# Performance work log

Measured on AMD Instinct MI355X. Metric: run time of the kernel, lower is better.

## Reference

```python
import jax, jax.numpy as jnp
import numpy as np

NEG = -100.0
M2M, M2I, M2D, I2M, I2I, D2M, D2D = range(7)
LOG_Q = float(np.log(0.25))


def _d_chain(fM, aM2D, aD2D):
    """Sequential delete-state recurrence along motif axis k.
    fD[k] = logaddexp(aM2D[k-1] + fM[k-1], aD2D[k-1] + fD[k-1]), fD[0] = NEG.
    fM: (B, K+1); aM2D, aD2D: (B, K+1). Returns (B, K+1)."""
    B, Kp1 = fM.shape
    K = Kp1 - 1

    def step(fd_prev, inp):
        am, ad, fm = inp  # each (B,)
        fd = jnp.logaddexp(am + fm, ad + fd_prev)
        return fd, fd

    init = jnp.full((B,), NEG, dtype=fM.dtype)
    _, fds = jax.lax.scan(step, init, (aM2D[:, :K].T, aD2D[:, :K].T, fM[:, :K].T))
    return jnp.concatenate([init[:, None], fds.T], axis=1)


def _profile_hmm_loss(a, e, x):
    """pHMM forward algorithm (log-space). a: (B,K+1,7), e: (B,K,4), x: (B,L) int.
    Returns -log P(x) per batch element, shape (B,)."""
    B, Kp1, _ = a.shape
    K = Kp1 - 1

    fM0 = jnp.full((B, Kp1), NEG, dtype=a.dtype).at[:, 0].set(0.0)
    fI0 = jnp.full((B, Kp1), NEG, dtype=a.dtype)
    fD0 = _d_chain(fM0, a[:, :, M2D], a[:, :, D2D])

    def l_step(carry, x_l):
        fM, fI, fD = carry
        # emission for symbol x_l at each match state k: (B, K)
        esel = jnp.take_along_axis(e, x_l[:, None, None].astype(jnp.int32), axis=2)[:, :, 0]
        prev = jnp.logaddexp(
            jnp.logaddexp(a[:, :K, M2M] + fM[:, :K], a[:, :K, I2M] + fI[:, :K]),
            a[:, :K, D2M] + fD[:, :K],
        )
        fM_new = jnp.concatenate([jnp.full((B, 1), NEG, dtype=a.dtype), esel + prev], axis=1)
        fI_new = LOG_Q + jnp.logaddexp(a[:, :, M2I] + fM, a[:, :, I2I] + fI)
        fD_new = _d_chain(fM_new, a[:, :, M2D], a[:, :, D2D])
        return (fM_new, fI_new, fD_new), None

    (fM, fI, fD), _ = jax.lax.scan(l_step, (fM0, fI0, fD0), x.T)

    final = jnp.stack(
        [fM[:, K] + a[:, K, M2M], fI[:, K] + a[:, K, I2M], fD[:, K] + a[:, K, D2M]],
        axis=1,
    )
    return -jax.nn.logsumexp(final, axis=1)


def _kld_loss(mus, logvars):
    return -0.5 * jnp.sum(1.0 + logvars - mus * mus - jnp.exp(logvars), axis=1)


def setup_inputs() -> dict:
    key = jax.random.key(0)
    k1, k2, k3, k4, k5 = jax.random.split(key, 5)
    B, K, L, E = 4096, 64, 128, 16
    batch_input = jax.random.randint(k1, (B, L), 0, 4, dtype=jnp.int32)
    transition_probs = jax.random.normal(k2, (B, K + 1, 7), dtype=jnp.float32)
    emission_probs = jax.random.normal(k3, (B, K, 4), dtype=jnp.float32)
    mus = jax.random.normal(k4, (B, E), dtype=jnp.float32)
    logvars = jax.random.normal(k5, (B, E), dtype=jnp.float32)
    return {
        "batch_input": batch_input,
        "transition_probs": transition_probs,
        "emission_probs": emission_probs,
        "mus": mus,
        "logvars": logvars,
    }


def reference(batch_input, transition_probs, emission_probs, mus, logvars):
    beta = 1.0
    recon = jnp.mean(_profile_hmm_loss(transition_probs, emission_probs, batch_input))
    kld = jnp.mean(_kld_loss(mus, logvars))
    return recon + beta * kld
```

## Files before the change

### kernel.cpp

```cpp
#include <hip/hip_runtime.h>
#include <math.h>


namespace {

constexpr float kLog2e = 1.4426950408889634f;
constexpr float kLn2   = 0.6931471805599453f;

__device__ __forceinline__ float fexp(float x) {
    return __builtin_amdgcn_exp2f(x * kLog2e);
}

template <int CTRL, bool BC>
__device__ __forceinline__ float dppf(float old, float src) {
    int r = __builtin_amdgcn_update_dpp(__builtin_bit_cast(int, old),
                                        __builtin_bit_cast(int, src),
                                        CTRL, 0xF, 0xF, BC);
    return __builtin_bit_cast(float, r);
}

__global__ __launch_bounds__(256) void phmm_vae_kernel(
    const int* __restrict__ xg,
    const float* __restrict__ ag,
    const float* __restrict__ eg,
    const float* __restrict__ mug,
    const float* __restrict__ lvg,
    float* __restrict__ out, unsigned* __restrict__ wsc, float* __restrict__ wsf,
    int B)
{
    const int tid  = threadIdx.x;
    const int lane = tid & 63;
    const int wv   = tid >> 6;
    const int b    = (blockIdx.x << 2) + wv;

    __shared__ float part[4];
    float contrib = 0.0f;

    if (b < B) {
        const float* ab = ag + (size_t)b * (65 * 7);
        const float* eb = eg + (size_t)b * (64 * 4);
        const int*   xb = xg + (size_t)b * 128;

        const int j = lane;
        const float AjM2D  = fexp(ab[j * 7 + 2]);
        const float d      = fexp(ab[j * 7 + 6]);
        const float A1M2M  = fexp(ab[(j + 1) * 7 + 0]);
        const float QA1M2I = 0.25f * fexp(ab[(j + 1) * 7 + 1]);
        const float A1I2M  = fexp(ab[(j + 1) * 7 + 3]);
        const float QA1I2I = 0.25f * fexp(ab[(j + 1) * 7 + 4]);
        const float A1D2M  = fexp(ab[(j + 1) * 7 + 5]);
        const float A0M2M  = fexp(ab[0]);
        const float QA0M2I = 0.25f * fexp(ab[1]);
        const float A0I2M  = fexp(ab[3]);
        const float D0     = 0.25f * fexp(ab[4]);

        float4 ev = *reinterpret_cast<const float4*>(eb + j * 4);
        const float E0 = fexp(ev.x), E1 = fexp(ev.y);
        const float E2 = fexp(ev.z), E3 = fexp(ev.w);

        const int xlo = xb[lane];
        const int xhi = xb[64 + lane];
        const unsigned long long b0lo = __ballot(xlo & 1);
        const unsigned long long b1lo = __ballot(xlo & 2);
        const unsigned long long b0hi = __ballot(xhi & 1);
        const unsigned long long b1hi = __ballot(xhi & 2);

        const float V1 = d;
        const float V2 = V1 * dppf<0x111, false>(1.0f, V1);
        const float V4 = V2 * dppf<0x112, false>(1.0f, V2);
        const float V8 = V4 * dppf<0x114, false>(1.0f, V4);
        float Q = d;
        Q *= dppf<0x111, false>(1.0f, Q);
        Q *= dppf<0x112, false>(1.0f, Q);
        Q *= dppf<0x114, false>(1.0f, Q);
        Q *= dppf<0x118, false>(1.0f, Q);
        const int   row  = lane >> 4;
        const float Q47  = __shfl(Q, 47, 64);
        const float QmA  = (row == 1 || row == 3) ? Q : 0.0f;
        const float QmB  = (row == 2) ? Q : ((row == 3) ? Q * Q47 : 0.0f);

        auto dchain = [&](float fMn, float f0) -> float {
            float fMp = dppf<0x138, false>(f0, fMn);
            float y = AjM2D * fMp;
            y = fmaf(V1,  dppf<0x111, true>(y, y), y);
            y = fmaf(V2,  dppf<0x112, true>(y, y), y);
            y = fmaf(V4,  dppf<0x114, true>(y, y), y);
            y = fmaf(V8,  dppf<0x118, true>(y, y), y);
            y = fmaf(QmA, dppf<0x142, true>(y, y), y);
            y = fmaf(QmB, dppf<0x143, true>(y, y), y);
            return y;
        };

        auto esel_of = [&](unsigned long long m0, unsigned long long m1,
                           int sh) -> float {
            int bit0 = (int)(m0 >> sh) & 1;
            int bit1 = (int)(m1 >> sh) & 1;
            float eA = bit0 ? E1 : E0;
            float eB = bit0 ? E3 : E2;
            return bit1 ? eB : eA;
        };

        float fM = 0.0f, fI = 0.0f;
        float fD = dchain(0.0f, 1.0f);
        float LS = 0.0f;
        float fI0v;

        auto stepf = [&](float esel, float p0) {
            float pl = fmaf(A1M2M, fM, fmaf(A1I2M, fI, A1D2M * fD));
            float prev = dppf<0x138, false>(p0, pl);
            float fMn = esel * prev;
            fI = fmaf(QA1M2I, fM, QA1I2I * fI);
            fD = dchain(fMn, 0.0f);
            fM = fMn;
        };

        auto rescale = [&]() {
            float m = fmaxf(fmaxf(fM, fI), fD);
            m = fmaxf(m, dppf<0xB1,  true>(m, m));
            m = fmaxf(m, dppf<0x4E,  true>(m, m));
            m = fmaxf(m, dppf<0x141, true>(m, m));
            m = fmaxf(m, dppf<0x140, true>(m, m));
            int mb = __builtin_bit_cast(int, m);
            unsigned u0 = (unsigned)__builtin_amdgcn_readlane(mb, 0);
            unsigned u1 = (unsigned)__builtin_amdgcn_readlane(mb, 16);
            unsigned u2 = (unsigned)__builtin_amdgcn_readlane(mb, 32);
            unsigned u3 = (unsigned)__builtin_amdgcn_readlane(mb, 48);
            unsigned ua = u0 > u1 ? u0 : u1;
            unsigned ub = u2 > u3 ? u2 : u3;
            unsigned um = ua > ub ? ua : ub;
            int ee = (int)(um >> 23);
            float r = __builtin_bit_cast(float, (unsigned)(254 - ee) << 23);
            LS += (float)(ee - 127);
            fM *= r; fI *= r; fD *= r; fI0v *= r;
        };

        stepf(esel_of(b0lo, b1lo, 0), A0M2M);
        fI0v = QA0M2I;

        for (int l = 1; l < 64; ++l) {
            stepf(esel_of(b0lo, b1lo, l), A0I2M * fI0v);
            fI0v *= D0;
            if ((l & 7) == 7) rescale();
        }
        for (int l = 64; l < 128; ++l) {
            stepf(esel_of(b0hi, b1hi, l - 64), A0I2M * fI0v);
            fI0v *= D0;
            if ((l & 7) == 7) rescale();
        }

        float F = fmaf(A1M2M, fM, fmaf(A1I2M, fI, A1D2M * fD));
        float loss = -(__builtin_amdgcn_logf(F) + LS) * kLn2;

        float kt = 0.0f;
        if (lane < 16) {
            float mu = mug[(size_t)b * 16 + lane];
            float lv = lvg[(size_t)b * 16 + lane];
            kt = 1.0f + lv - mu * mu - fexp(lv);
        }
        kt += __shfl_xor(kt, 1, 64);
        kt += __shfl_xor(kt, 2, 64);
        kt += __shfl_xor(kt, 4, 64);
        kt += __shfl_xor(kt, 8, 64);
        float kldb = __shfl(-0.5f * kt, 0, 64);

        contrib = (loss + kldb) * (1.0f / 4096.0f);
    }

    if (lane == 63) part[wv] = (b < B) ? contrib : 0.0f;
    __syncthreads();
    if (tid == 0) {
        float bs = part[0] + part[1] + part[2] + part[3];
        const float    poisonf = __builtin_bit_cast(float, 0xAAAAAAAAu);
        atomicAdd(&wsf[1], bs);
        __threadfence();
        unsigned old = atomicAdd(&wsc[0], 1u);
        if (old == 0xAAAAAAAAu + (unsigned)(gridDim.x - 1)) {
            __threadfence();
            float total = atomicAdd(&wsf[1], 0.0f);
            out[0] = total - poisonf;
        }
    }
}

}

extern "C" void kernel_launch(void* const* d_in, const int* in_sizes, int n_in,
                              void* d_out, int out_size, void* d_ws, size_t ws_size,
                              hipStream_t stream) {
    const int*   x  = (const int*)d_in[0];
    const float* a  = (const float*)d_in[1];
    const float* e  = (const float*)d_in[2];
    const float* mu = (const float*)d_in[3];
    const float* lv = (const float*)d_in[4];
    float* out = (float*)d_out;

    const int B = in_sizes[0] / 128;
    const int grid = (B + 3) / 4;

    phmm_vae_kernel<<<grid, 256, 0, stream>>>(x, a, e, mu, lv, out,
                                              (unsigned*)d_ws, (float*)d_ws, B);
}
```

Measured before the change: 110.1 us.

## Fold delete-chain into match recurrence with inline-asm DPP scan and two-kernel reduction

Reformulates the per-step recurrence so the delete-state scan acts on the previous match input, with emissions and the M2D weight premultiplied into per-symbol constants. This takes the dchain off the dependency path between steps and carries the combined next-step value `pl` instead. The prefix scan is written as inline assembly with fused DPP multiply/fma ops, and lane masks are built into the scan coefficients. The atomic-counter final reduction is replaced by per-block partial sums plus a second tiny reduce kernel, which adds a kernel launch and relies on hand-placed s_nop hazards.

```diff
diff --git a/kernel.cpp b/kernel.cpp
--- a/kernel.cpp
+++ b/kernel.cpp
@@ -25,8 +25,7 @@
     const float* __restrict__ eg,
     const float* __restrict__ mug,
     const float* __restrict__ lvg,
-    float* __restrict__ out, unsigned* __restrict__ wsc, float* __restrict__ wsf,
-    int B)
+    float* __restrict__ partials, int B)
 {
     const int tid  = threadIdx.x;
     const int lane = tid & 63;
@@ -42,13 +41,13 @@
         const int*   xb = xg + (size_t)b * 128;
 
         const int j = lane;
-        const float AjM2D  = fexp(ab[j * 7 + 2]);
-        const float d      = fexp(ab[j * 7 + 6]);
+        const float a2  = ab[j * 7 + 2];
+        const float a6  = ab[j * 7 + 6];
+        const float a5  = ab[(j + 1) * 7 + 5];
         const float A1M2M  = fexp(ab[(j + 1) * 7 + 0]);
         const float QA1M2I = 0.25f * fexp(ab[(j + 1) * 7 + 1]);
         const float A1I2M  = fexp(ab[(j + 1) * 7 + 3]);
         const float QA1I2I = 0.25f * fexp(ab[(j + 1) * 7 + 4]);
-        const float A1D2M  = fexp(ab[(j + 1) * 7 + 5]);
         const float A0M2M  = fexp(ab[0]);
         const float QA0M2I = 0.25f * fexp(ab[1]);
         const float A0I2M  = fexp(ab[3]);
@@ -65,91 +64,110 @@
         const unsigned long long b0hi = __ballot(xhi & 1);
         const unsigned long long b1hi = __ballot(xhi & 2);
 
-        const float V1 = d;
+        const float a5p = dppf<0x138, false>(0.0f, a5);
+        const float dh  = fexp(a6 + a5 - a5p);
+        const float wM2D = fexp(a2 + a5);
+        const float C0 = wM2D * dppf<0x138, false>(0.0f, E0);
+        const float C1 = wM2D * dppf<0x138, false>(0.0f, E1);
+        const float C2 = wM2D * dppf<0x138, false>(0.0f, E2);
+        const float C3 = wM2D * dppf<0x138, false>(0.0f, E3);
+
+        const float V1 = dh;
         const float V2 = V1 * dppf<0x111, false>(1.0f, V1);
         const float V4 = V2 * dppf<0x112, false>(1.0f, V2);
         const float V8 = V4 * dppf<0x114, false>(1.0f, V4);
-        float Q = d;
+        const float V1m = (lane >= 1)  ? V1 : 0.0f;
+        const float V2m = (lane >= 2)  ? V2 : 0.0f;
+        const float V4m = (lane >= 4)  ? V4 : 0.0f;
+        const float V8m = (lane >= 8)  ? V8 : 0.0f;
+        float Q = dh;
         Q *= dppf<0x111, false>(1.0f, Q);
         Q *= dppf<0x112, false>(1.0f, Q);
         Q *= dppf<0x114, false>(1.0f, Q);
         Q *= dppf<0x118, false>(1.0f, Q);
-        const int   row  = lane >> 4;
-        const float Q47  = __shfl(Q, 47, 64);
-        const float QmA  = (row == 1 || row == 3) ? Q : 0.0f;
-        const float QmB  = (row == 2) ? Q : ((row == 3) ? Q * Q47 : 0.0f);
-
-        auto dchain = [&](float fMn, float f0) -> float {
-            float fMp = dppf<0x138, false>(f0, fMn);
-            float y = AjM2D * fMp;
-            y = fmaf(V1,  dppf<0x111, true>(y, y), y);
-            y = fmaf(V2,  dppf<0x112, true>(y, y), y);
-            y = fmaf(V4,  dppf<0x114, true>(y, y), y);
-            y = fmaf(V8,  dppf<0x118, true>(y, y), y);
-            y = fmaf(QmA, dppf<0x142, true>(y, y), y);
-            y = fmaf(QmB, dppf<0x143, true>(y, y), y);
+        const int   row = lane >> 4;
+        const float Q47 = __shfl(Q, 47, 64);
+        const float QmA = (row == 1 || row == 3) ? Q : 0.0f;
+        const float QmB = (row == 2) ? Q : ((row == 3) ? Q * Q47 : 0.0f);
+
+        auto scan_asm = [&](float prev, float Cs) -> float {
+            float y;
+            asm("s_nop 1\n\t"
+                "v_mul_f32_dpp %0, %1, %2 wave_shr:1 row_mask:0xf bank_mask:0xf bound_ctrl:0\n\t"
+                "s_nop 1\n\t"
+                "v_fmac_f32_dpp %0, %0, %3 row_shr:1 row_mask:0xf bank_mask:0xf bound_ctrl:0\n\t"
+                "s_nop 1\n\t"
+                "v_fmac_f32_dpp %0, %0, %4 row_shr:2 row_mask:0xf bank_mask:0xf bound_ctrl:0\n\t"
+                "s_nop 1\n\t"
+                "v_fmac_f32_dpp %0, %0, %5 row_shr:4 row_mask:0xf bank_mask:0xf bound_ctrl:0\n\t"
+                "s_nop 1\n\t"
+                "v_fmac_f32_dpp %0, %0, %6 row_shr:8 row_mask:0xf bank_mask:0xf bound_ctrl:0\n\t"
+                "s_nop 1\n\t"
+                "v_fmac_f32_dpp %0, %0, %7 row_bcast:15 row_mask:0xf bank_mask:0xf bound_ctrl:0\n\t"
+                "s_nop 1\n\t"
+                "v_fmac_f32_dpp %0, %0, %8 row_bcast:31 row_mask:0xf bank_mask:0xf bound_ctrl:0"
+                : "=&v"(y)
+                : "v"(prev), "v"(Cs), "v"(V1m), "v"(V2m), "v"(V4m), "v"(V8m),
+                  "v"(QmA), "v"(QmB));
             return y;
         };
 
-        auto esel_of = [&](unsigned long long m0, unsigned long long m1,
-                           int sh) -> float {
-            int bit0 = (int)(m0 >> sh) & 1;
-            int bit1 = (int)(m1 >> sh) & 1;
-            float eA = bit0 ? E1 : E0;
-            float eB = bit0 ? E3 : E2;
-            return bit1 ? eB : eA;
-        };
+        float y0 = (lane == 0) ? wM2D : 0.0f;
+        y0 = fmaf(V1m, dppf<0x111, true>(0.0f, y0), y0);
+        y0 = fmaf(V2m, dppf<0x112, true>(0.0f, y0), y0);
+        y0 = fmaf(V4m, dppf<0x114, true>(0.0f, y0), y0);
+        y0 = fmaf(V8m, dppf<0x118, true>(0.0f, y0), y0);
+        y0 = fmaf(QmA, dppf<0x142, true>(0.0f, y0), y0);
+        y0 = fmaf(QmB, dppf<0x143, true>(0.0f, y0), y0);
 
         float fM = 0.0f, fI = 0.0f;
-        float fD = dchain(0.0f, 1.0f);
+        float pl = y0;
+        float fI0v = 0.0f;
         float LS = 0.0f;
-        float fI0v;
-
-        auto stepf = [&](float esel, float p0) {
-            float pl = fmaf(A1M2M, fM, fmaf(A1I2M, fI, A1D2M * fD));
-            float prev = dppf<0x138, false>(p0, pl);
-            float fMn = esel * prev;
+
+#pragma unroll 8
+        for (int l = 0; l < 128; ++l) {
+            const unsigned long long m0 = (l < 64) ? b0lo : b0hi;
+            const unsigned long long m1 = (l < 64) ? b1lo : b1hi;
+            const int sh = l & 63;
+            const int bit0 = (int)(m0 >> sh) & 1;
+            const int bit1 = (int)(m1 >> sh) & 1;
+            const float Es = bit1 ? (bit0 ? E3 : E2) : (bit0 ? E1 : E0);
+            const float Cs = bit1 ? (bit0 ? C3 : C2) : (bit0 ? C1 : C0);
+
+            const float p0v = (l == 0) ? A0M2M : A0I2M * fI0v;
+            const float prev = dppf<0x138, false>(p0v, pl);
+            const float fMn = Es * prev;
+            const float z = scan_asm(prev, Cs);
             fI = fmaf(QA1M2I, fM, QA1I2I * fI);
-            fD = dchain(fMn, 0.0f);
             fM = fMn;
-        };
-
-        auto rescale = [&]() {
-            float m = fmaxf(fmaxf(fM, fI), fD);
-            m = fmaxf(m, dppf<0xB1,  true>(m, m));
-            m = fmaxf(m, dppf<0x4E,  true>(m, m));
-            m = fmaxf(m, dppf<0x141, true>(m, m));
-            m = fmaxf(m, dppf<0x140, true>(m, m));
-            int mb = __builtin_bit_cast(int, m);
-            unsigned u0 = (unsigned)__builtin_amdgcn_readlane(mb, 0);
-            unsigned u1 = (unsigned)__builtin_amdgcn_readlane(mb, 16);
-            unsigned u2 = (unsigned)__builtin_amdgcn_readlane(mb, 32);
-            unsigned u3 = (unsigned)__builtin_amdgcn_readlane(mb, 48);
-            unsigned ua = u0 > u1 ? u0 : u1;
-            unsigned ub = u2 > u3 ? u2 : u3;
-            unsigned um = ua > ub ? ua : ub;
-            int ee = (int)(um >> 23);
-            float r = __builtin_bit_cast(float, (unsigned)(254 - ee) << 23);
-            LS += (float)(ee - 127);
-            fM *= r; fI *= r; fD *= r; fI0v *= r;
-        };
-
-        stepf(esel_of(b0lo, b1lo, 0), A0M2M);
-        fI0v = QA0M2I;
-
-        for (int l = 1; l < 64; ++l) {
-            stepf(esel_of(b0lo, b1lo, l), A0I2M * fI0v);
-            fI0v *= D0;
-            if ((l & 7) == 7) rescale();
+            pl = fmaf(A1M2M, fM, fmaf(A1I2M, fI, z));
+            fI0v = (l == 0) ? QA0M2I : fI0v * D0;
+
+            if ((l & 7) == 7) {
+                float m = fmaxf(fmaxf(fM, fI), pl);
+                m = fmaxf(m, dppf<0xB1,  true>(0.0f, m));
+                m = fmaxf(m, dppf<0x4E,  true>(0.0f, m));
+                m = fmaxf(m, dppf<0x141, true>(0.0f, m));
+                m = fmaxf(m, dppf<0x140, true>(0.0f, m));
+                m = fmaxf(m, 1e-35f);
+                int mb = __builtin_bit_cast(int, m);
+                unsigned u0 = (unsigned)__builtin_amdgcn_readlane(mb, 0);
+                unsigned u1 = (unsigned)__builtin_amdgcn_readlane(mb, 16);
+                unsigned u2 = (unsigned)__builtin_amdgcn_readlane(mb, 32);
+                unsigned u3 = (unsigned)__builtin_amdgcn_readlane(mb, 48);
+                unsigned ua = u0 > u1 ? u0 : u1;
+                unsigned ub = u2 > u3 ? u2 : u3;
+                unsigned um = ua > ub ? ua : ub;
+                int ee = (int)(um >> 23);
+                float r = __builtin_bit_cast(float, (unsigned)(254 - ee) << 23);
+                LS += (float)(ee - 127);
+                fM *= r; fI *= r; pl *= r; fI0v *= r;
+            }
         }
-        for (int l = 64; l < 128; ++l) {
-            stepf(esel_of(b0hi, b1hi, l - 64), A0I2M * fI0v);
-            fI0v *= D0;
-            if ((l & 7) == 7) rescale();
-        }
-
-        float F = fmaf(A1M2M, fM, fmaf(A1I2M, fI, A1D2M * fD));
-        float loss = -(__builtin_amdgcn_logf(F) + LS) * kLn2;
+
+        const float Fv = __shfl(pl, 63, 64);
+        const float loss = -(__builtin_amdgcn_logf(Fv) + LS) * kLn2;
 
         float kt = 0.0f;
         if (lane < 16) {
@@ -169,17 +187,26 @@
     if (lane == 63) part[wv] = (b < B) ? contrib : 0.0f;
     __syncthreads();
     if (tid == 0) {
-        float bs = part[0] + part[1] + part[2] + part[3];
-        const float    poisonf = __builtin_bit_cast(float, 0xAAAAAAAAu);
-        atomicAdd(&wsf[1], bs);
-        __threadfence();
-        unsigned old = atomicAdd(&wsc[0], 1u);
-        if (old == 0xAAAAAAAAu + (unsigned)(gridDim.x - 1)) {
-            __threadfence();
-            float total = atomicAdd(&wsf[1], 0.0f);
-            out[0] = total - poisonf;
-        }
+        partials[blockIdx.x] = part[0] + part[1] + part[2] + part[3];
     }
+}
+
+__global__ __launch_bounds__(256) void reduce_kernel(
+    const float* __restrict__ p, float* __restrict__ out, int n)
+{
+    const int tid = threadIdx.x;
+    float s = 0.0f;
+    for (int i = tid; i < n; i += 256) s += p[i];
+    s += __shfl_xor(s, 1, 64);
+    s += __shfl_xor(s, 2, 64);
+    s += __shfl_xor(s, 4, 64);
+    s += __shfl_xor(s, 8, 64);
+    s += __shfl_xor(s, 16, 64);
+    s += __shfl_xor(s, 32, 64);
+    __shared__ float ps[4];
+    if ((tid & 63) == 0) ps[tid >> 6] = s;
+    __syncthreads();
+    if (tid == 0) out[0] = ps[0] + ps[1] + ps[2] + ps[3];
 }
 
 }
@@ -193,10 +220,11 @@
     const float* mu = (const float*)d_in[3];
     const float* lv = (const float*)d_in[4];
     float* out = (float*)d_out;
+    float* partials = (float*)d_ws;
 
     const int B = in_sizes[0] / 128;
     const int grid = (B + 3) / 4;
 
-    phmm_vae_kernel<<<grid, 256, 0, stream>>>(x, a, e, mu, lv, out,
-                                              (unsigned*)d_ws, (float*)d_ws, B);
-}
+    phmm_vae_kernel<<<grid, 256, 0, stream>>>(x, a, e, mu, lv, partials, B);
+    reduce_kernel<<<1, 256, 0, stream>>>(partials, out, grid);
+}
```

Result: faster. 95.62 us (-13.1%).
